# Performance work log

Measured on AMD Instinct MI355X. Metric: run time of the kernel, lower is better.

## Reference

```python
import jax, jax.numpy as jnp
import numpy as np

B, T, I, H = 65536, 9, 57, 2  # batch, seq_len, input_size, hidden_size


def setup_inputs() -> dict:
    key = jax.random.key(0)
    ks = jax.random.split(key, 7)
    return {
        "x": jax.random.normal(ks[0], (B, T, I), dtype=jnp.float32),
        "W_ih": jax.random.normal(ks[1], (4 * H, I), dtype=jnp.float32) * 0.1,
        "W_hh": jax.random.normal(ks[2], (4 * H, H), dtype=jnp.float32) * 0.1,
        "b_ih": jax.random.normal(ks[3], (4 * H,), dtype=jnp.float32) * 0.1,
        "b_hh": jax.random.normal(ks[4], (4 * H,), dtype=jnp.float32) * 0.1,
        "fc_w": jax.random.normal(ks[5], (1, H), dtype=jnp.float32) * 0.1,
        "fc_b": jax.random.normal(ks[6], (1,), dtype=jnp.float32) * 0.1,
    }


def reference(x, W_ih, W_hh, b_ih, b_hh, fc_w, fc_b):
    # Precompute input contribution to the gates for all timesteps: [B, T, 4H]
    gx = jnp.einsum("bti,gi->btg", x, W_ih) + b_ih + b_hh
    h0 = jnp.zeros((x.shape[0], W_hh.shape[1]), dtype=x.dtype)
    c0 = jnp.zeros_like(h0)

    def step(carry, g_t):
        h, c = carry
        g = g_t + h @ W_hh.T  # [B, 4H]
        i, f, gg, o = jnp.split(g, 4, axis=-1)  # PyTorch gate order: i, f, g, o
        i = jax.nn.sigmoid(i)
        f = jax.nn.sigmoid(f)
        gg = jnp.tanh(gg)
        o = jax.nn.sigmoid(o)
        c = f * c + i * gg
        h = o * jnp.tanh(c)
        return (h, c), None

    (h_T, _), _ = jax.lax.scan(step, (h0, c0), jnp.swapaxes(gx, 0, 1))  # scan over time
    # fc applied to last hidden state: [B, 1]
    return h_T @ fc_w.T + fc_b
```

## Files before the change

kernel.cpp:

```cpp
#include <hip/hip_runtime.h>


#define B_TOTAL 65536
#define T_STEPS 9
#define I_DIM   57
#define BATCH_PER_BLOCK 64
#define ROWS_PER_BLOCK (BATCH_PER_BLOCK * T_STEPS)
#define ROWS_PER_WAVE  (ROWS_PER_BLOCK / 4)
#define WCHUNK_ROWS 8
#define N_WCHUNKS   (ROWS_PER_WAVE / WCHUNK_ROWS)
#define WCHUNK_DW   (WCHUNK_ROWS * I_DIM)
#define WCHUNK_F4   (WCHUNK_DW / 4)
#define GX_PAD      9
#define NBLOCKS     (B_TOTAL / BATCH_PER_BLOCK)

__device__ __forceinline__ float fast_tanh(float v) {
    float e = __builtin_amdgcn_exp2f(2.885390082f * v);
    return 1.0f - 2.0f * __builtin_amdgcn_rcpf(e + 1.0f);
}
__device__ __forceinline__ float fast_sig(float v) {
    return 0.5f * fast_tanh(0.5f * v) + 0.5f;
}

#define DPP_ROR_F32(VAR, SRC, CTRL)                                          \
    float VAR = __builtin_bit_cast(float, __builtin_amdgcn_update_dpp(       \
        0, __builtin_bit_cast(int, SRC), (CTRL), 0xF, 0xF, false))

__global__ __launch_bounds__(256, 4)
void lstm_onepass(const float* __restrict__ x,
                  const float* __restrict__ W_ih,
                  const float* __restrict__ W_hh,
                  const float* __restrict__ b_ih,
                  const float* __restrict__ b_hh,
                  const float* __restrict__ fc_w,
                  const float* __restrict__ fc_b,
                  float* __restrict__ out) {
    __shared__ float xs[4][2][WCHUNK_DW];
    __shared__ float gxp[ROWS_PER_BLOCK * GX_PAD];

    const int tid  = threadIdx.x;
    const int wv   = tid >> 6;
    const int lane = tid & 63;
    const int cl   = (lane >> 4) & 3;
    const int g    = (lane >> 1) & 7;
    const int p    = lane & 1;
    const int rin  = cl * 2 + p;

    float wrot[8][8];
#pragma unroll
    for (int d = 0; d < 8; ++d) {
        const int gg = (g + d) & 7;
        const float* wr = W_ih + gg * I_DIM;
#pragma unroll
        for (int k = 0; k < 7; ++k) wrot[d][k] = wr[g + 8 * k];
        wrot[d][7] = (g == 0) ? wr[56] : 0.0f;
    }
    float bsum = b_ih[g] + b_hh[g];
#pragma unroll
    for (int d = 0; d < 8; ++d)
#pragma unroll
        for (int k = 0; k < 8; ++k)
            asm volatile("" : "+v"(wrot[d][k]));

    const float* xw = x + (size_t)blockIdx.x * (ROWS_PER_BLOCK * I_DIM)
                        + (size_t)wv * (ROWS_PER_WAVE * I_DIM);

    float4 st0, st1;

#define STAGE_LOAD(C) do {                                                  \
        const float4* xc_ = (const float4*)(xw + (size_t)(C) * WCHUNK_DW);  \
        st0 = xc_[lane];                                                    \
        if (lane < WCHUNK_F4 - 64) st1 = xc_[64 + lane];                    \
    } while (0)

#define STAGE_WRITE(S) do {                                                 \
        float4* L_ = (float4*)xs[wv][S];                                    \
        L_[lane] = st0;                                                     \
        if (lane < WCHUNK_F4 - 64) L_[64 + lane] = st1;                     \
    } while (0)

#define COMPUTE(S, C) do {                                                  \
        const float* row_ = xs[wv][S] + rin * I_DIM;                        \
        float xv_[8];                                                       \
        _Pragma("unroll")                                                   \
        for (int k = 0; k < 7; ++k) xv_[k] = row_[g + 8 * k];               \
        xv_[7] = row_[56];            \
        float acc_[8];                                                      \
        _Pragma("unroll")                                                   \
        for (int d = 0; d < 8; ++d) {                                       \
            float s_ = wrot[d][0] * xv_[0];                                 \
            _Pragma("unroll")                                               \
            for (int k = 1; k < 8; ++k) s_ += wrot[d][k] * xv_[k];          \
            acc_[d] = s_;                                                   \
        }                                                                   \
                       \
        DPP_ROR_F32(r1_, acc_[1], 0x122);                                   \
        DPP_ROR_F32(r2_, acc_[2], 0x124);                                   \
        DPP_ROR_F32(r3_, acc_[3], 0x126);                                   \
        DPP_ROR_F32(r4_, acc_[4], 0x128);                                   \
        DPP_ROR_F32(r5_, acc_[5], 0x12A);                                   \
        DPP_ROR_F32(r6_, acc_[6], 0x12C);                                   \
        DPP_ROR_F32(r7_, acc_[7], 0x12E);                                   \
        float tot_ = ((acc_[0] + r1_) + (r2_ + r3_))                        \
                   + ((r4_ + r5_) + (r6_ + r7_)) + bsum;                    \
        gxp[(wv * ROWS_PER_WAVE + (C) * WCHUNK_ROWS + rin) * GX_PAD + g]    \
            = tot_;                                                         \
    } while (0)

    STAGE_LOAD(0);
    STAGE_WRITE(0);
    STAGE_LOAD(1);

#pragma unroll
    for (int cc = 0; cc < N_WCHUNKS; ++cc) {
        COMPUTE(cc & 1, cc);
        if (cc + 1 < N_WCHUNKS) STAGE_WRITE((cc + 1) & 1);
        if (cc + 2 < N_WCHUNKS) STAGE_LOAD(cc + 2);
    }
#undef STAGE_LOAD
#undef STAGE_WRITE
#undef COMPUTE

    if (lane < 16) {
        float w0[8], w1[8];
#pragma unroll
        for (int q = 0; q < 8; ++q) {
            w0[q] = W_hh[q * 2];
            w1[q] = W_hh[q * 2 + 1];
        }

        const int bloc = wv * 16 + lane;
        float h0 = 0.f, h1 = 0.f, c0 = 0.f, c1 = 0.f;
        const float* gb = gxp + bloc * (T_STEPS * GX_PAD);

#pragma unroll
        for (int t = 0; t < T_STEPS; ++t) {
            const float* pp = gb + t * GX_PAD;
            const float i0 = fast_sig (pp[0] + h0 * w0[0] + h1 * w1[0]);
            const float i1 = fast_sig (pp[1] + h0 * w0[1] + h1 * w1[1]);
            const float f0 = fast_sig (pp[2] + h0 * w0[2] + h1 * w1[2]);
            const float f1 = fast_sig (pp[3] + h0 * w0[3] + h1 * w1[3]);
            const float g0 = fast_tanh(pp[4] + h0 * w0[4] + h1 * w1[4]);
            const float g1 = fast_tanh(pp[5] + h0 * w0[5] + h1 * w1[5]);
            const float o0 = fast_sig (pp[6] + h0 * w0[6] + h1 * w1[6]);
            const float o1 = fast_sig (pp[7] + h0 * w0[7] + h1 * w1[7]);
            c0 = f0 * c0 + i0 * g0;
            c1 = f1 * c1 + i1 * g1;
            h0 = o0 * fast_tanh(c0);
            h1 = o1 * fast_tanh(c1);
        }

        out[blockIdx.x * BATCH_PER_BLOCK + bloc] =
            h0 * fc_w[0] + h1 * fc_w[1] + fc_b[0];
    }
}

extern "C" void kernel_launch(void* const* d_in, const int* in_sizes, int n_in,
                              void* d_out, int out_size, void* d_ws, size_t ws_size,
                              hipStream_t stream) {
    const float* x    = (const float*)d_in[0];
    const float* W_ih = (const float*)d_in[1];
    const float* W_hh = (const float*)d_in[2];
    const float* b_ih = (const float*)d_in[3];
    const float* b_hh = (const float*)d_in[4];
    const float* fc_w = (const float*)d_in[5];
    const float* fc_b = (const float*)d_in[6];
    float* out = (float*)d_out;

    lstm_onepass<<<dim3(NBLOCKS), dim3(256), 0, stream>>>(
        x, W_ih, W_hh, b_ih, b_hh, fc_w, fc_b, out);
}
```

Before: 39.25 us.

## Deepen global prefetch to three register stages and drop padded weight column

Replaces the single register staging buffer with three rotating register stages, so global loads for chunk cc+3 are issued while chunk cc is computed. This puts more memory requests in flight to hide HBM latency. It also drops the mostly zero eighth weight column and handles element 56 with one separate multiply-add per lane. That frees registers and removes wasted FMAs. The extra staging registers raise VGPR pressure and could lower occupancy under the 4-waves launch bound.

```diff
diff --git a/kernel.cpp b/kernel.cpp
--- a/kernel.cpp
+++ b/kernel.cpp
@@ -46,51 +46,52 @@
     const int p    = lane & 1;
     const int rin  = cl * 2 + p;
 
-    float wrot[8][8];
+    float wrot[8][7];
 #pragma unroll
     for (int d = 0; d < 8; ++d) {
         const int gg = (g + d) & 7;
         const float* wr = W_ih + gg * I_DIM;
 #pragma unroll
         for (int k = 0; k < 7; ++k) wrot[d][k] = wr[g + 8 * k];
-        wrot[d][7] = (g == 0) ? wr[56] : 0.0f;
     }
+    float w56  = W_ih[g * I_DIM + 56];
     float bsum = b_ih[g] + b_hh[g];
 #pragma unroll
     for (int d = 0; d < 8; ++d)
 #pragma unroll
-        for (int k = 0; k < 8; ++k)
+        for (int k = 0; k < 7; ++k)
             asm volatile("" : "+v"(wrot[d][k]));
+    asm volatile("" : "+v"(w56), "+v"(bsum));
 
     const float* xw = x + (size_t)blockIdx.x * (ROWS_PER_BLOCK * I_DIM)
                         + (size_t)wv * (ROWS_PER_WAVE * I_DIM);
 
-    float4 st0, st1;
+    float4 s0a, s0b, s1a, s1b, s2a, s2b;
 
-#define STAGE_LOAD(C) do {                                                  \
+#define SLOAD(C, RA, RB) do {                                               \
         const float4* xc_ = (const float4*)(xw + (size_t)(C) * WCHUNK_DW);  \
-        st0 = xc_[lane];                                                    \
-        if (lane < WCHUNK_F4 - 64) st1 = xc_[64 + lane];                    \
+        RA = xc_[lane];                                                     \
+        if (lane < WCHUNK_F4 - 64) RB = xc_[64 + lane];                     \
     } while (0)
 
-#define STAGE_WRITE(S) do {                                                 \
+#define SWRITE(S, RA, RB) do {                                              \
         float4* L_ = (float4*)xs[wv][S];                                    \
-        L_[lane] = st0;                                                     \
-        if (lane < WCHUNK_F4 - 64) L_[64 + lane] = st1;                     \
+        L_[lane] = RA;                                                      \
+        if (lane < WCHUNK_F4 - 64) L_[64 + lane] = RB;                      \
     } while (0)
 
 #define COMPUTE(S, C) do {                                                  \
         const float* row_ = xs[wv][S] + rin * I_DIM;                        \
-        float xv_[8];                                                       \
+        float xv_[7];                                                       \
         _Pragma("unroll")                                                   \
         for (int k = 0; k < 7; ++k) xv_[k] = row_[g + 8 * k];               \
-        xv_[7] = row_[56];            \
+        const float x56_ = row_[56];            \
         float acc_[8];                                                      \
         _Pragma("unroll")                                                   \
         for (int d = 0; d < 8; ++d) {                                       \
             float s_ = wrot[d][0] * xv_[0];                                 \
             _Pragma("unroll")                                               \
-            for (int k = 1; k < 8; ++k) s_ += wrot[d][k] * xv_[k];          \
+            for (int k = 1; k < 7; ++k) s_ += wrot[d][k] * xv_[k];          \
             acc_[d] = s_;                                                   \
         }                                                                   \
                        \
@@ -102,23 +103,33 @@
         DPP_ROR_F32(r6_, acc_[6], 0x12C);                                   \
         DPP_ROR_F32(r7_, acc_[7], 0x12E);                                   \
         float tot_ = ((acc_[0] + r1_) + (r2_ + r3_))                        \
-                   + ((r4_ + r5_) + (r6_ + r7_)) + bsum;                    \
+                   + ((r4_ + r5_) + (r6_ + r7_))                            \
+                   + bsum + w56 * x56_;                                     \
         gxp[(wv * ROWS_PER_WAVE + (C) * WCHUNK_ROWS + rin) * GX_PAD + g]    \
             = tot_;                                                         \
     } while (0)
 
-    STAGE_LOAD(0);
-    STAGE_WRITE(0);
-    STAGE_LOAD(1);
+    SLOAD(0, s0a, s0b);
+    SLOAD(1, s1a, s1b);
+    SLOAD(2, s2a, s2b);
+    SWRITE(0, s0a, s0b);
 
 #pragma unroll
     for (int cc = 0; cc < N_WCHUNKS; ++cc) {
         COMPUTE(cc & 1, cc);
-        if (cc + 1 < N_WCHUNKS) STAGE_WRITE((cc + 1) & 1);
-        if (cc + 2 < N_WCHUNKS) STAGE_LOAD(cc + 2);
+        if (cc + 3 < N_WCHUNKS) {
+            if      (cc % 3 == 0) SLOAD(cc + 3, s0a, s0b);
+            else if (cc % 3 == 1) SLOAD(cc + 3, s1a, s1b);
+            else                  SLOAD(cc + 3, s2a, s2b);
+        }
+        if (cc + 1 < N_WCHUNKS) {
+            if      ((cc + 1) % 3 == 0) SWRITE((cc + 1) & 1, s0a, s0b);
+            else if ((cc + 1) % 3 == 1) SWRITE((cc + 1) & 1, s1a, s1b);
+            else                        SWRITE((cc + 1) & 1, s2a, s2b);
+        }
     }
-#undef STAGE_LOAD
-#undef STAGE_WRITE
+#undef SLOAD
+#undef SWRITE
 #undef COMPUTE
 
     if (lane < 16) {
```

Result: faster. 37.65 us (-4.1%).
